# Optimization experiments

Measured on AMD Instinct MI355X. Metric: run time of the kernel, lower is better.

Reference implementation:

```python
import jax, jax.numpy as jnp
import numpy as np
import math

D_MODEL = 1024
NUM_HEADS = 16
HEAD_DIM = D_MODEL // NUM_HEADS


def _sinusoidal_pe(seq_len, dim, dtype=jnp.float32):
    # Matches RotaryPositionEmbedding buffer: pe[:,0::2]=sin, pe[:,1::2]=cos
    pos = jnp.arange(seq_len, dtype=jnp.float32)[:, None]            # [S,1]
    div = jnp.exp(jnp.arange(0, dim, 2, dtype=jnp.float32) * (-math.log(10000.0) / dim))  # [dim/2]
    ang = pos * div[None, :]                                          # [S,dim/2]
    pe = jnp.stack([jnp.sin(ang), jnp.cos(ang)], axis=-1).reshape(seq_len, dim)
    return pe.astype(dtype)


def setup_inputs() -> dict:
    key = jax.random.key(0)
    ks = jax.random.split(key, 11)
    B, S, D = 4, 1024, D_MODEL
    s = 1.0 / math.sqrt(D)
    inp = {
        "q": jax.random.normal(ks[0], (B, S, D), jnp.float32),
        "k": jax.random.normal(ks[1], (B, S, D), jnp.float32),
        "v": jax.random.normal(ks[2], (B, S, D), jnp.float32),
        "Wq": jax.random.normal(ks[3], (D, D), jnp.float32) * s,
        "bq": jax.random.normal(ks[4], (D,), jnp.float32) * s,
        "Wk": jax.random.normal(ks[5], (D, D), jnp.float32) * s,
        "bk": jax.random.normal(ks[6], (D,), jnp.float32) * s,
        "Wv": jax.random.normal(ks[7], (D, D), jnp.float32) * s,
        "bv": jax.random.normal(ks[8], (D,), jnp.float32) * s,
        "Wo": jax.random.normal(ks[9], (D, D), jnp.float32) * s,
        "bo": jax.random.normal(ks[10], (D,), jnp.float32) * s,
    }
    return inp


def reference(q, k, v, Wq, bq, Wk, bk, Wv, bv, Wo, bo):
    B, S, D = q.shape
    H, hd = NUM_HEADS, HEAD_DIM
    scale = hd ** -0.5

    def proj(x, W, b):  # nn.Linear: x @ W.T + b, then [B,H,S,hd]
        return (x @ W.T + b).reshape(B, S, H, hd).transpose(0, 2, 1, 3)

    qh = proj(q, Wq, bq)
    kh = proj(k, Wk, bk)
    vh = proj(v, Wv, bv)

    pe = _sinusoidal_pe(S, hd, qh.dtype)[None, None]  # [1,1,S,hd]
    qh = qh + pe
    kh = kh + pe

    scores = jnp.einsum("bhqd,bhkd->bhqk", qh, kh) * scale  # [B,H,S,S]
    attn = jax.nn.softmax(scores, axis=-1)
    out = jnp.einsum("bhqk,bhkd->bhqd", attn, vh)            # [B,H,S,hd]
    out = out.transpose(0, 2, 1, 3).reshape(B, S, D)
    return out @ Wo.T + bo
```

## Files before the change

kernel.cpp:

```cpp
#include <hip/hip_runtime.h>
#include <hip/hip_bf16.h>

#define B_  4
#define S_  1024
#define D_  1024
#define H_  16
#define HD_ 64

typedef __bf16 bf16;
typedef __bf16 bf16x8 __attribute__((ext_vector_type(8)));
typedef __bf16 bf16x4 __attribute__((ext_vector_type(4)));
typedef float  f32x4  __attribute__((ext_vector_type(4)));

__device__ __forceinline__ void gll16(const void* g, void* l) {
    __builtin_amdgcn_global_load_lds((__attribute__((address_space(1))) void*)(void*)g,
                                     (__attribute__((address_space(3))) void*)l,
                                     16, 0, 0);
}

__global__ __launch_bounds__(256)
void convert_w_kernel(const float* __restrict__ Wq, const float* __restrict__ Wk,
                      const float* __restrict__ Wv, const float* __restrict__ Wo,
                      bf16* __restrict__ dst)
{
    const int idx   = blockIdx.x * 256 + threadIdx.x;
    const int which = idx >> 17;
    const int off   = (idx & 131071) * 8;
    const float* s  = (which == 0) ? Wq : (which == 1) ? Wk : (which == 2) ? Wv : Wo;
    const f32x4 a = *(const f32x4*)(s + off);
    const f32x4 b = *(const f32x4*)(s + off + 4);
    bf16x8 o;
#pragma unroll
    for (int jj = 0; jj < 4; ++jj) { o[jj] = (bf16)a[jj]; o[jj + 4] = (bf16)b[jj]; }
    *(bf16x8*)(dst + ((size_t)which << 20) + off) = o;
}

__global__ __launch_bounds__(256)
void qkv_proj_kernel(const float* __restrict__ qin, const float* __restrict__ kin,
                     const float* __restrict__ vin,
                     const bf16* __restrict__ Wall,
                     const float* __restrict__ bq, const float* __restrict__ bk,
                     const float* __restrict__ bv,
                     bf16* __restrict__ Qh, bf16* __restrict__ Kh,
                     bf16* __restrict__ Vt)
{
    __shared__ __align__(16) bf16 sA[128 * 32];
    __shared__ __align__(16) bf16 sB[128 * 32];

    const int z = blockIdx.z;
    const float* __restrict__ X    = (z == 0) ? qin : (z == 1) ? kin : vin;
    const float* __restrict__ bias = (z == 0) ? bq  : (z == 1) ? bk  : bv;

    const int m0   = blockIdx.y * 128;
    const int n0   = blockIdx.x * 128;
    const int tid  = threadIdx.x;
    const int lane = tid & 63;
    const int wave = tid >> 6;
    const int lr   = lane & 15;
    const int lg   = lane >> 4;
    const int mw   = (wave >> 1) * 64;
    const int nw   = (wave & 1) * 64;
    const int srow = tid >> 2;
    const int skg  = (tid & 3) * 8;

    f32x4 acc[4][4];
#pragma unroll
    for (int i = 0; i < 4; ++i)
#pragma unroll
        for (int j = 0; j < 4; ++j) acc[i][j] = (f32x4){0.f, 0.f, 0.f, 0.f};

    const float* Ab = X + (size_t)(m0 + srow) * D_ + skg;
    const bf16*  Wb = Wall + ((size_t)z << 20) + (size_t)(n0 + srow) * D_ + skg;

    for (int kt = 0; kt < 32; ++kt) {
        const int k0 = kt * 32;
        f32x4 ga[2][2];
#pragma unroll
        for (int p = 0; p < 2; ++p) {
            const float* ar = Ab + (size_t)(p * 64) * D_ + k0;
            ga[p][0] = *(const f32x4*)(ar);
            ga[p][1] = *(const f32x4*)(ar + 4);
        }
        __syncthreads();
#pragma unroll
        for (int p = 0; p < 2; ++p)
            gll16(Wb + (size_t)(p * 64) * D_ + k0, (char*)sB + p * 4096 + tid * 16);
#pragma unroll
        for (int p = 0; p < 2; ++p) {
            bf16x8 ta;
#pragma unroll
            for (int jj = 0; jj < 4; ++jj) {
                ta[jj]     = (bf16)ga[p][0][jj];
                ta[jj + 4] = (bf16)ga[p][1][jj];
            }
            *(bf16x8*)(sA + p * 2048 + tid * 8) = ta;
        }
        __syncthreads();

        bf16x8 af[4], bfr[4];
#pragma unroll
        for (int i = 0; i < 4; ++i)
            af[i] = *(const bf16x8*)(sA + (mw + 16 * i + lr) * 32 + lg * 8);
#pragma unroll
        for (int j = 0; j < 4; ++j)
            bfr[j] = *(const bf16x8*)(sB + (nw + 16 * j + lr) * 32 + lg * 8);
#pragma unroll
        for (int i = 0; i < 4; ++i)
#pragma unroll
            for (int j = 0; j < 4; ++j)
                acc[i][j] = __builtin_amdgcn_mfma_f32_16x16x32_bf16(af[i], bfr[j],
                                                                    acc[i][j], 0, 0, 0);
    }

    if (z < 2) {
        bf16* dst = (z == 0) ? Qh : Kh;
#pragma unroll
        for (int i = 0; i < 4; ++i) {
#pragma unroll
            for (int j = 0; j < 4; ++j) {
                const int n = n0 + nw + 16 * j + lr;
                const int h = n >> 6, d = n & 63;
                const float bn = bias[n];
                const float dv_rev = 0.15915494309189535f *
                    exp2f(-(float)(d & ~1) * 0.20762050593046648f);
#pragma unroll
                for (int r = 0; r < 4; ++r) {
                    const int m = m0 + mw + 16 * i + lg * 4 + r;
                    const int b = m >> 10, s = m & 1023;
                    float rev = (float)s * dv_rev;
                    rev -= floorf(rev);
                    const float sv = __builtin_amdgcn_sinf(rev);
                    const float cv = __builtin_amdgcn_cosf(rev);
                    const float pe  = (d & 1) ? cv : sv;
                    const float val = acc[i][j][r] + bn + pe;
                    dst[(size_t)((b * H_ + h) * S_ + s) * HD_ + d] = (bf16)val;
                }
            }
        }
    } else {
#pragma unroll
        for (int i = 0; i < 4; ++i) {
            const int mb = m0 + mw + 16 * i + lg * 4;
            const int b = mb >> 10, sb = mb & 1023;
#pragma unroll
            for (int j = 0; j < 4; ++j) {
                const int n = n0 + nw + 16 * j + lr;
                const int h = n >> 6, d = n & 63;
                const float bn = bias[n];
                bf16x4 pk;
#pragma unroll
                for (int r = 0; r < 4; ++r) pk[r] = (bf16)(acc[i][j][r] + bn);
                *(bf16x4*)(Vt + (size_t)((b * H_ + h) * HD_ + d) * S_ + sb) = pk;
            }
        }
    }
}

#define LDK 72
__global__ __launch_bounds__(128)
void attn_kernel(const bf16* __restrict__ Qh, const bf16* __restrict__ Kh,
                 const bf16* __restrict__ Vt, bf16* __restrict__ att)
{
    __shared__ __align__(16) bf16 sK[64 * LDK];
    __shared__ __align__(16) bf16 sV[64 * LDK];
    __shared__ __align__(16) bf16 sP[2 * 32 * LDK];

    const int tid  = threadIdx.x;
    const int lane = tid & 63;
    const int wave = tid >> 6;
    const int lr   = lane & 15;
    const int lg   = lane >> 4;
    const int bh   = blockIdx.y;
    const int qw   = blockIdx.x * 64 + wave * 32;

    const bf16* Qb = Qh + (size_t)bh * S_ * HD_;
    const bf16* Kb = Kh + (size_t)bh * S_ * HD_;
    const bf16* Vb = Vt + (size_t)bh * HD_ * S_;

    bf16x8 qa[2][2];
#pragma unroll
    for (int i = 0; i < 2; ++i)
#pragma unroll
        for (int ks = 0; ks < 2; ++ks)
            qa[i][ks] = *(const bf16x8*)(Qb + (size_t)(qw + 16 * i + lr) * HD_ +
                                         ks * 32 + lg * 8);

    f32x4 o[2][4];
    float lsum[2][4];
#pragma unroll
    for (int i = 0; i < 2; ++i) {
#pragma unroll
        for (int jd = 0; jd < 4; ++jd) o[i][jd] = (f32x4){0.f, 0.f, 0.f, 0.f};
#pragma unroll
        for (int r = 0; r < 4; ++r) lsum[i][r] = 0.f;
    }

    bf16* const pw   = sP + wave * 32 * LDK;
    const int  srow  = tid >> 3;
    const int  scol  = (tid & 7) * 8;

    for (int kc = 0; kc < 16; ++kc) {
        bf16x8 kv[4], vv[4];
#pragma unroll
        for (int p = 0; p < 4; ++p) {
            kv[p] = *(const bf16x8*)(Kb + (size_t)(kc * 64 + p * 16 + srow) * HD_ + scol);
            vv[p] = *(const bf16x8*)(Vb + (size_t)(p * 16 + srow) * S_ + kc * 64 + scol);
        }
        __syncthreads();
#pragma unroll
        for (int p = 0; p < 4; ++p) {
            *(bf16x8*)(sK + (p * 16 + srow) * LDK + scol) = kv[p];
            *(bf16x8*)(sV + (p * 16 + srow) * LDK + scol) = vv[p];
        }
        __syncthreads();

        bf16x8 kb[4][2];
#pragma unroll
        for (int jk = 0; jk < 4; ++jk)
#pragma unroll
            for (int ks = 0; ks < 2; ++ks)
                kb[jk][ks] = *(const bf16x8*)(sK + (16 * jk + lr) * LDK + ks * 32 + lg * 8);

#pragma unroll
        for (int i = 0; i < 2; ++i)
#pragma unroll
            for (int jk = 0; jk < 4; ++jk) {
                f32x4 s = (f32x4){0.f, 0.f, 0.f, 0.f};
                s = __builtin_amdgcn_mfma_f32_16x16x32_bf16(qa[i][0], kb[jk][0], s, 0, 0, 0);
                s = __builtin_amdgcn_mfma_f32_16x16x32_bf16(qa[i][1], kb[jk][1], s, 0, 0, 0);
#pragma unroll
                for (int r = 0; r < 4; ++r) {
                    const float pp = __expf(s[r] * 0.125f);
                    lsum[i][r] += pp;
                    pw[(16 * i + lg * 4 + r) * LDK + 16 * jk + lr] = (bf16)pp;
                }
            }
        asm volatile("s_waitcnt lgkmcnt(0)" ::: "memory");

#pragma unroll
        for (int ks = 0; ks < 2; ++ks) {
            bf16x8 pa[2];
#pragma unroll
            for (int i = 0; i < 2; ++i)
                pa[i] = *(const bf16x8*)(pw + (16 * i + lr) * LDK + ks * 32 + lg * 8);
#pragma unroll
            for (int jd = 0; jd < 4; ++jd) {
                const bf16x8 vb = *(const bf16x8*)(sV + (16 * jd + lr) * LDK +
                                                   ks * 32 + lg * 8);
#pragma unroll
                for (int i = 0; i < 2; ++i)
                    o[i][jd] = __builtin_amdgcn_mfma_f32_16x16x32_bf16(pa[i], vb,
                                                                       o[i][jd], 0, 0, 0);
            }
        }
    }

    const int b = bh >> 4, h = bh & 15;
#pragma unroll
    for (int i = 0; i < 2; ++i)
#pragma unroll
        for (int r = 0; r < 4; ++r) {
            float l = lsum[i][r];
#pragma unroll
            for (int off = 1; off < 16; off <<= 1)
                l += __shfl_xor(l, off, 64);
            const float inv = 1.f / l;
            const int s = qw + 16 * i + lg * 4 + r;
#pragma unroll
            for (int jd = 0; jd < 4; ++jd) {
                const int d = 16 * jd + lr;
                att[(size_t)(b * S_ + s) * D_ + h * HD_ + d] = (bf16)(o[i][jd][r] * inv);
            }
        }
}

__global__ __launch_bounds__(256)
void out_proj_kernel(const bf16* __restrict__ A, const bf16* __restrict__ Wob,
                     const float* __restrict__ bo, float* __restrict__ out)
{
    __shared__ __align__(16) bf16 sA[128 * 32];
    __shared__ __align__(16) bf16 sB[128 * 32];

    const int m0   = blockIdx.y * 128;
    const int n0   = blockIdx.x * 128;
    const int tid  = threadIdx.x;
    const int lane = tid & 63;
    const int wave = tid >> 6;
    const int lr   = lane & 15;
    const int lg   = lane >> 4;
    const int mw   = (wave >> 1) * 64;
    const int nw   = (wave & 1) * 64;
    const int srow = tid >> 2;
    const int skg  = (tid & 3) * 8;

    f32x4 acc[4][4];
#pragma unroll
    for (int i = 0; i < 4; ++i)
#pragma unroll
        for (int j = 0; j < 4; ++j) acc[i][j] = (f32x4){0.f, 0.f, 0.f, 0.f};

    const bf16* Ab = A   + (size_t)(m0 + srow) * D_ + skg;
    const bf16* Wb = Wob + (size_t)(n0 + srow) * D_ + skg;

    for (int kt = 0; kt < 32; ++kt) {
        const int k0 = kt * 32;
        __syncthreads();
#pragma unroll
        for (int p = 0; p < 2; ++p) {
            gll16(Ab + (size_t)(p * 64) * D_ + k0, (char*)sA + p * 4096 + tid * 16);
            gll16(Wb + (size_t)(p * 64) * D_ + k0, (char*)sB + p * 4096 + tid * 16);
        }
        __syncthreads();

        bf16x8 af[4], bfr[4];
#pragma unroll
        for (int i = 0; i < 4; ++i)
            af[i] = *(const bf16x8*)(sA + (mw + 16 * i + lr) * 32 + lg * 8);
#pragma unroll
        for (int j = 0; j < 4; ++j)
            bfr[j] = *(const bf16x8*)(sB + (nw + 16 * j + lr) * 32 + lg * 8);
#pragma unroll
        for (int i = 0; i < 4; ++i)
#pragma unroll
            for (int j = 0; j < 4; ++j)
                acc[i][j] = __builtin_amdgcn_mfma_f32_16x16x32_bf16(af[i], bfr[j],
                                                                    acc[i][j], 0, 0, 0);
    }

#pragma unroll
    for (int i = 0; i < 4; ++i)
#pragma unroll
        for (int j = 0; j < 4; ++j) {
            const int n = n0 + nw + 16 * j + lr;
            const float bn = bo[n];
#pragma unroll
            for (int r = 0; r < 4; ++r) {
                const int m = m0 + mw + 16 * i + lg * 4 + r;
                out[(size_t)m * D_ + n] = acc[i][j][r] + bn;
            }
        }
}

extern "C" void kernel_launch(void* const* d_in, const int* in_sizes, int n_in,
                              void* d_out, int out_size, void* d_ws, size_t ws_size,
                              hipStream_t stream)
{
    const float* q  = (const float*)d_in[0];
    const float* k  = (const float*)d_in[1];
    const float* v  = (const float*)d_in[2];
    const float* Wq = (const float*)d_in[3];
    const float* bq = (const float*)d_in[4];
    const float* Wk = (const float*)d_in[5];
    const float* bk = (const float*)d_in[6];
    const float* Wv = (const float*)d_in[7];
    const float* bv = (const float*)d_in[8];
    const float* Wo = (const float*)d_in[9];
    const float* bo = (const float*)d_in[10];

    char* ws = (char*)d_ws;
    const size_t SZ = (size_t)B_ * H_ * S_ * HD_ * sizeof(bf16);
    bf16* Qh  = (bf16*)(ws);
    bf16* Kh  = (bf16*)(ws + SZ);
    bf16* Vt  = (bf16*)(ws + 2 * SZ);
    bf16* att = (bf16*)(ws + 3 * SZ);

    bf16* Wall = (bf16*)d_out;

    convert_w_kernel<<<2048, 256, 0, stream>>>(Wq, Wk, Wv, Wo, Wall);
    qkv_proj_kernel<<<dim3(8, 32, 3), 256, 0, stream>>>(q, k, v, Wall, bq, bk, bv,
                                                        Qh, Kh, Vt);
    attn_kernel<<<dim3(16, 64), 128, 0, stream>>>(Qh, Kh, Vt, att);
    hipMemcpyAsync((void*)Qh, (const void*)(Wall + ((size_t)3 << 20)),
                   (size_t)D_ * D_ * sizeof(bf16), hipMemcpyDeviceToDevice, stream);
    out_proj_kernel<<<dim3(8, 32), 256, 0, stream>>>(att, (const bf16*)Qh, bo,
                                                     (float*)d_out);
}
```

Measured before the change: 233.1 us.

## Fuse weight conversion into GEMMs, prefetch tiles, fold softmax scale, retile grids

Removes the separate fp32-to-bf16 weight conversion kernel and the device memcpy. The QKV and output projection GEMMs now load fp32 weights directly, convert them in registers, and software-prefetch the next K tile while the current one is computed. The attention kernel now uses 256 threads per block with register prefetch of K/V chunks. The 1/sqrt(hd) scale is folded into the Q projection epilogue, and the grids are linearised with M-fastest block ordering. The output projection uses 64-row tiles to launch more blocks. Reading fp32 weights doubles weight traffic per tile, and prefetching raises register pressure.

```diff
diff --git a/kernel.cpp b/kernel.cpp
--- a/kernel.cpp
+++ b/kernel.cpp
@@ -12,33 +12,18 @@
 typedef __bf16 bf16x4 __attribute__((ext_vector_type(4)));
 typedef float  f32x4  __attribute__((ext_vector_type(4)));
 
-__device__ __forceinline__ void gll16(const void* g, void* l) {
-    __builtin_amdgcn_global_load_lds((__attribute__((address_space(1))) void*)(void*)g,
-                                     (__attribute__((address_space(3))) void*)l,
-                                     16, 0, 0);
-}
-
-__global__ __launch_bounds__(256)
-void convert_w_kernel(const float* __restrict__ Wq, const float* __restrict__ Wk,
-                      const float* __restrict__ Wv, const float* __restrict__ Wo,
-                      bf16* __restrict__ dst)
-{
-    const int idx   = blockIdx.x * 256 + threadIdx.x;
-    const int which = idx >> 17;
-    const int off   = (idx & 131071) * 8;
-    const float* s  = (which == 0) ? Wq : (which == 1) ? Wk : (which == 2) ? Wv : Wo;
-    const f32x4 a = *(const f32x4*)(s + off);
-    const f32x4 b = *(const f32x4*)(s + off + 4);
+__device__ __forceinline__ bf16x8 pack8(const f32x4 a, const f32x4 b) {
     bf16x8 o;
 #pragma unroll
     for (int jj = 0; jj < 4; ++jj) { o[jj] = (bf16)a[jj]; o[jj + 4] = (bf16)b[jj]; }
-    *(bf16x8*)(dst + ((size_t)which << 20) + off) = o;
+    return o;
 }
 
 __global__ __launch_bounds__(256)
 void qkv_proj_kernel(const float* __restrict__ qin, const float* __restrict__ kin,
                      const float* __restrict__ vin,
-                     const bf16* __restrict__ Wall,
+                     const float* __restrict__ Wq, const float* __restrict__ Wk,
+                     const float* __restrict__ Wv,
                      const float* __restrict__ bq, const float* __restrict__ bk,
                      const float* __restrict__ bv,
                      bf16* __restrict__ Qh, bf16* __restrict__ Kh,
@@ -47,12 +32,17 @@
     __shared__ __align__(16) bf16 sA[128 * 32];
     __shared__ __align__(16) bf16 sB[128 * 32];
 
-    const int z = blockIdx.z;
+    const int blk  = blockIdx.x;
+    const int mIdx = blk & 31;
+    const int t    = blk >> 5;
+    const int nIdx = t & 7;
+    const int z    = t >> 3;
+
+    const int m0 = mIdx * 128, n0 = nIdx * 128;
     const float* __restrict__ X    = (z == 0) ? qin : (z == 1) ? kin : vin;
+    const float* __restrict__ W    = (z == 0) ? Wq  : (z == 1) ? Wk  : Wv;
     const float* __restrict__ bias = (z == 0) ? bq  : (z == 1) ? bk  : bv;
 
-    const int m0   = blockIdx.y * 128;
-    const int n0   = blockIdx.x * 128;
     const int tid  = threadIdx.x;
     const int lane = tid & 63;
     const int wave = tid >> 6;
@@ -70,32 +60,36 @@
         for (int j = 0; j < 4; ++j) acc[i][j] = (f32x4){0.f, 0.f, 0.f, 0.f};
 
     const float* Ab = X + (size_t)(m0 + srow) * D_ + skg;
-    const bf16*  Wb = Wall + ((size_t)z << 20) + (size_t)(n0 + srow) * D_ + skg;
+    const float* Wb = W + (size_t)(n0 + srow) * D_ + skg;
+
+    f32x4 ga[2][2], gw[2][2];
+#pragma unroll
+    for (int p = 0; p < 2; ++p) {
+        const float* ar = Ab + (size_t)(p * 64) * D_;
+        const float* wr = Wb + (size_t)(p * 64) * D_;
+        ga[p][0] = *(const f32x4*)(ar);  ga[p][1] = *(const f32x4*)(ar + 4);
+        gw[p][0] = *(const f32x4*)(wr);  gw[p][1] = *(const f32x4*)(wr + 4);
+    }
 
     for (int kt = 0; kt < 32; ++kt) {
-        const int k0 = kt * 32;
-        f32x4 ga[2][2];
+        __syncthreads();
 #pragma unroll
         for (int p = 0; p < 2; ++p) {
-            const float* ar = Ab + (size_t)(p * 64) * D_ + k0;
-            ga[p][0] = *(const f32x4*)(ar);
-            ga[p][1] = *(const f32x4*)(ar + 4);
-        }
-        __syncthreads();
-#pragma unroll
-        for (int p = 0; p < 2; ++p)
-            gll16(Wb + (size_t)(p * 64) * D_ + k0, (char*)sB + p * 4096 + tid * 16);
-#pragma unroll
-        for (int p = 0; p < 2; ++p) {
-            bf16x8 ta;
-#pragma unroll
-            for (int jj = 0; jj < 4; ++jj) {
-                ta[jj]     = (bf16)ga[p][0][jj];
-                ta[jj + 4] = (bf16)ga[p][1][jj];
-            }
-            *(bf16x8*)(sA + p * 2048 + tid * 8) = ta;
-        }
-        __syncthreads();
+            *(bf16x8*)(sA + p * 2048 + tid * 8) = pack8(ga[p][0], ga[p][1]);
+            *(bf16x8*)(sB + p * 2048 + tid * 8) = pack8(gw[p][0], gw[p][1]);
+        }
+        __syncthreads();
+
+        if (kt < 31) {
+            const int k1 = (kt + 1) * 32;
+#pragma unroll
+            for (int p = 0; p < 2; ++p) {
+                const float* ar = Ab + (size_t)(p * 64) * D_ + k1;
+                const float* wr = Wb + (size_t)(p * 64) * D_ + k1;
+                ga[p][0] = *(const f32x4*)(ar);  ga[p][1] = *(const f32x4*)(ar + 4);
+                gw[p][0] = *(const f32x4*)(wr);  gw[p][1] = *(const f32x4*)(wr + 4);
+            }
+        }
 
         bf16x8 af[4], bfr[4];
 #pragma unroll
@@ -114,6 +108,7 @@
 
     if (z < 2) {
         bf16* dst = (z == 0) ? Qh : Kh;
+        const float sc = (z == 0) ? 0.125f : 1.0f;
 #pragma unroll
         for (int i = 0; i < 4; ++i) {
 #pragma unroll
@@ -132,7 +127,7 @@
                     const float sv = __builtin_amdgcn_sinf(rev);
                     const float cv = __builtin_amdgcn_cosf(rev);
                     const float pe  = (d & 1) ? cv : sv;
-                    const float val = acc[i][j][r] + bn + pe;
+                    const float val = (acc[i][j][r] + bn + pe) * sc;
                     dst[(size_t)((b * H_ + h) * S_ + s) * HD_ + d] = (bf16)val;
                 }
             }
@@ -157,21 +152,22 @@
 }
 
 #define LDK 72
-__global__ __launch_bounds__(128)
+__global__ __launch_bounds__(256)
 void attn_kernel(const bf16* __restrict__ Qh, const bf16* __restrict__ Kh,
                  const bf16* __restrict__ Vt, bf16* __restrict__ att)
 {
     __shared__ __align__(16) bf16 sK[64 * LDK];
     __shared__ __align__(16) bf16 sV[64 * LDK];
-    __shared__ __align__(16) bf16 sP[2 * 32 * LDK];
+    __shared__ __align__(16) bf16 sP[4 * 32 * LDK];
 
     const int tid  = threadIdx.x;
     const int lane = tid & 63;
     const int wave = tid >> 6;
     const int lr   = lane & 15;
     const int lg   = lane >> 4;
-    const int bh   = blockIdx.y;
-    const int qw   = blockIdx.x * 64 + wave * 32;
+    const int bh   = blockIdx.x & 63;
+    const int qt   = blockIdx.x >> 6;
+    const int qw   = qt * 128 + wave * 32;
 
     const bf16* Qb = Qh + (size_t)bh * S_ * HD_;
     const bf16* Kb = Kh + (size_t)bh * S_ * HD_;
@@ -199,20 +195,30 @@
     const int  srow  = tid >> 3;
     const int  scol  = (tid & 7) * 8;
 
+    bf16x8 kv[2], vv[2];
+#pragma unroll
+    for (int p = 0; p < 2; ++p) {
+        kv[p] = *(const bf16x8*)(Kb + (size_t)(p * 32 + srow) * HD_ + scol);
+        vv[p] = *(const bf16x8*)(Vb + (size_t)(p * 32 + srow) * S_ + scol);
+    }
+
     for (int kc = 0; kc < 16; ++kc) {
-        bf16x8 kv[4], vv[4];
-#pragma unroll
-        for (int p = 0; p < 4; ++p) {
-            kv[p] = *(const bf16x8*)(Kb + (size_t)(kc * 64 + p * 16 + srow) * HD_ + scol);
-            vv[p] = *(const bf16x8*)(Vb + (size_t)(p * 16 + srow) * S_ + kc * 64 + scol);
-        }
-        __syncthreads();
-#pragma unroll
-        for (int p = 0; p < 4; ++p) {
-            *(bf16x8*)(sK + (p * 16 + srow) * LDK + scol) = kv[p];
-            *(bf16x8*)(sV + (p * 16 + srow) * LDK + scol) = vv[p];
-        }
-        __syncthreads();
+        __syncthreads();
+#pragma unroll
+        for (int p = 0; p < 2; ++p) {
+            *(bf16x8*)(sK + (p * 32 + srow) * LDK + scol) = kv[p];
+            *(bf16x8*)(sV + (p * 32 + srow) * LDK + scol) = vv[p];
+        }
+        __syncthreads();
+
+        if (kc < 15) {
+            const int kn = (kc + 1) * 64;
+#pragma unroll
+            for (int p = 0; p < 2; ++p) {
+                kv[p] = *(const bf16x8*)(Kb + (size_t)(kn + p * 32 + srow) * HD_ + scol);
+                vv[p] = *(const bf16x8*)(Vb + (size_t)(p * 32 + srow) * S_ + kn + scol);
+            }
+        }
 
         bf16x8 kb[4][2];
 #pragma unroll
@@ -230,7 +236,7 @@
                 s = __builtin_amdgcn_mfma_f32_16x16x32_bf16(qa[i][1], kb[jk][1], s, 0, 0, 0);
 #pragma unroll
                 for (int r = 0; r < 4; ++r) {
-                    const float pp = __expf(s[r] * 0.125f);
+                    const float pp = __expf(s[r]);
                     lsum[i][r] += pp;
                     pw[(16 * i + lg * 4 + r) * LDK + 16 * jk + lr] = (bf16)pp;
                 }
@@ -275,52 +281,72 @@
 }
 
 __global__ __launch_bounds__(256)
-void out_proj_kernel(const bf16* __restrict__ A, const bf16* __restrict__ Wob,
+void out_proj_kernel(const bf16* __restrict__ A, const float* __restrict__ Wo,
                      const float* __restrict__ bo, float* __restrict__ out)
 {
-    __shared__ __align__(16) bf16 sA[128 * 32];
+    __shared__ __align__(16) bf16 sA[64 * 32];
     __shared__ __align__(16) bf16 sB[128 * 32];
 
-    const int m0   = blockIdx.y * 128;
-    const int n0   = blockIdx.x * 128;
+    const int blk  = blockIdx.x;
+    const int mIdx = blk & 63;
+    const int nIdx = blk >> 6;
+    const int m0 = mIdx * 64, n0 = nIdx * 128;
+
     const int tid  = threadIdx.x;
     const int lane = tid & 63;
     const int wave = tid >> 6;
     const int lr   = lane & 15;
     const int lg   = lane >> 4;
-    const int mw   = (wave >> 1) * 64;
+    const int mw   = (wave >> 1) * 32;
     const int nw   = (wave & 1) * 64;
     const int srow = tid >> 2;
     const int skg  = (tid & 3) * 8;
 
-    f32x4 acc[4][4];
-#pragma unroll
-    for (int i = 0; i < 4; ++i)
+    f32x4 acc[2][4];
+#pragma unroll
+    for (int i = 0; i < 2; ++i)
 #pragma unroll
         for (int j = 0; j < 4; ++j) acc[i][j] = (f32x4){0.f, 0.f, 0.f, 0.f};
 
-    const bf16* Ab = A   + (size_t)(m0 + srow) * D_ + skg;
-    const bf16* Wb = Wob + (size_t)(n0 + srow) * D_ + skg;
+    const bf16*  Ab = A  + (size_t)(m0 + srow) * D_ + skg;
+    const float* Wb = Wo + (size_t)(n0 + srow) * D_ + skg;
+
+    bf16x8 aa;
+    f32x4  gw[2][2];
+    aa = *(const bf16x8*)(Ab);
+#pragma unroll
+    for (int p = 0; p < 2; ++p) {
+        const float* wr = Wb + (size_t)(p * 64) * D_;
+        gw[p][0] = *(const f32x4*)(wr);  gw[p][1] = *(const f32x4*)(wr + 4);
+    }
 
     for (int kt = 0; kt < 32; ++kt) {
-        const int k0 = kt * 32;
-        __syncthreads();
-#pragma unroll
-        for (int p = 0; p < 2; ++p) {
-            gll16(Ab + (size_t)(p * 64) * D_ + k0, (char*)sA + p * 4096 + tid * 16);
-            gll16(Wb + (size_t)(p * 64) * D_ + k0, (char*)sB + p * 4096 + tid * 16);
-        }
-        __syncthreads();
-
-        bf16x8 af[4], bfr[4];
-#pragma unroll
-        for (int i = 0; i < 4; ++i)
+        __syncthreads();
+        *(bf16x8*)(sA + tid * 8) = aa;
+#pragma unroll
+        for (int p = 0; p < 2; ++p)
+            *(bf16x8*)(sB + p * 2048 + tid * 8) = pack8(gw[p][0], gw[p][1]);
+        __syncthreads();
+
+        if (kt < 31) {
+            const int k1 = (kt + 1) * 32;
+            aa = *(const bf16x8*)(Ab + k1);
+#pragma unroll
+            for (int p = 0; p < 2; ++p) {
+                const float* wr = Wb + (size_t)(p * 64) * D_ + k1;
+                gw[p][0] = *(const f32x4*)(wr);  gw[p][1] = *(const f32x4*)(wr + 4);
+            }
+        }
+
+        bf16x8 af[2], bfr[4];
+#pragma unroll
+        for (int i = 0; i < 2; ++i)
             af[i] = *(const bf16x8*)(sA + (mw + 16 * i + lr) * 32 + lg * 8);
 #pragma unroll
         for (int j = 0; j < 4; ++j)
             bfr[j] = *(const bf16x8*)(sB + (nw + 16 * j + lr) * 32 + lg * 8);
 #pragma unroll
-        for (int i = 0; i < 4; ++i)
+        for (int i = 0; i < 2; ++i)
 #pragma unroll
             for (int j = 0; j < 4; ++j)
                 acc[i][j] = __builtin_amdgcn_mfma_f32_16x16x32_bf16(af[i], bfr[j],
@@ -328,7 +354,7 @@
     }
 
 #pragma unroll
-    for (int i = 0; i < 4; ++i)
+    for (int i = 0; i < 2; ++i)
 #pragma unroll
         for (int j = 0; j < 4; ++j) {
             const int n = n0 + nw + 16 * j + lr;
@@ -358,20 +384,14 @@
     const float* bo = (const float*)d_in[10];
 
     char* ws = (char*)d_ws;
-    const size_t SZ = (size_t)B_ * H_ * S_ * HD_ * sizeof(bf16);
+    const size_t MB8 = (size_t)8 * 1024 * 1024;
     bf16* Qh  = (bf16*)(ws);
-    bf16* Kh  = (bf16*)(ws + SZ);
-    bf16* Vt  = (bf16*)(ws + 2 * SZ);
-    bf16* att = (bf16*)(ws + 3 * SZ);
-
-    bf16* Wall = (bf16*)d_out;
-
-    convert_w_kernel<<<2048, 256, 0, stream>>>(Wq, Wk, Wv, Wo, Wall);
-    qkv_proj_kernel<<<dim3(8, 32, 3), 256, 0, stream>>>(q, k, v, Wall, bq, bk, bv,
-                                                        Qh, Kh, Vt);
-    attn_kernel<<<dim3(16, 64), 128, 0, stream>>>(Qh, Kh, Vt, att);
-    hipMemcpyAsync((void*)Qh, (const void*)(Wall + ((size_t)3 << 20)),
-                   (size_t)D_ * D_ * sizeof(bf16), hipMemcpyDeviceToDevice, stream);
-    out_proj_kernel<<<dim3(8, 32), 256, 0, stream>>>(att, (const bf16*)Qh, bo,
-                                                     (float*)d_out);
-}
+    bf16* Kh  = (bf16*)(ws + MB8);
+    bf16* Vt  = (bf16*)(ws + 2 * MB8);
+    bf16* att = (bf16*)(ws + 3 * MB8);
+
+    qkv_proj_kernel<<<768, 256, 0, stream>>>(q, k, v, Wq, Wk, Wv, bq, bk, bv,
+                                             Qh, Kh, Vt);
+    attn_kernel<<<512, 256, 0, stream>>>(Qh, Kh, Vt, att);
+    out_proj_kernel<<<512, 256, 0, stream>>>(att, Wo, bo, (float*)d_out);
+}
```

Result: no change. 232.5 us (-0.3%).
